# Optimization experiments

Measured on AMD Instinct MI355X. Metric: run time of the kernel, lower is better.

The kernel has to match this reference:

```python
import jax, jax.numpy as jnp
import numpy as np

N, C, T, V = 16, 128, 128, 25
K, H, OC = 3, 8, 256          # kernel_size subsets, heads, out_channels
HOPMAX = 12                   # hop values in [0, 12); emb_table size HOPMAX
EPS_BN = 1e-5
EPS_NORM = 1e-4


def setup_inputs() -> dict:
    key = jax.random.key(0)
    ks = jax.random.split(key, 12)
    s = 0.05
    x = jax.random.normal(ks[0], (N, C, T, V), jnp.float32)
    hop = jax.random.randint(ks[1], (V, V), 0, HOPMAX)
    emb_table = jax.random.normal(ks[2], (K, H, HOPMAX), jnp.float32) * s
    # A initialized as identity (as in the module) plus small noise for nontrivial grads
    A = jnp.tile(jnp.eye(V, dtype=jnp.float32), (K, H, 1, 1)) \
        + jax.random.normal(ks[3], (K, H, V, V), jnp.float32) * s
    w_block = jax.random.normal(ks[4], (K * OC, C // H), jnp.float32) * s  # grouped 1x1 conv, groups=K*H
    b_block = jax.random.normal(ks[5], (K * OC,), jnp.float32) * s
    bn_gamma = jnp.ones((OC,), jnp.float32)
    bn_beta = jnp.zeros((OC,), jnp.float32)
    res_w = jax.random.normal(ks[6], (OC, C), jnp.float32) * s  # residual 1x1 conv
    res_b = jax.random.normal(ks[7], (OC,), jnp.float32) * s
    res_bn_gamma = jnp.ones((OC,), jnp.float32)
    res_bn_beta = jnp.zeros((OC,), jnp.float32)
    return {"x": x, "hop": hop, "emb_table": emb_table, "A": A,
            "w_block": w_block, "b_block": b_block,
            "bn_gamma": bn_gamma, "bn_beta": bn_beta,
            "res_w": res_w, "res_b": res_b,
            "res_bn_gamma": res_bn_gamma, "res_bn_beta": res_bn_beta}


def _batchnorm(x, gamma, beta):
    # training-mode BatchNorm2d: batch stats over (N, T, V), biased variance
    m = jnp.mean(x, axis=(0, 2, 3), keepdims=True)
    v = jnp.var(x, axis=(0, 2, 3), keepdims=True)
    xn = (x - m) * jax.lax.rsqrt(v + EPS_BN)
    return gamma[None, :, None, None] * xn + beta[None, :, None, None]


def _l2_col_norm(w):
    # torch.norm(w, p=2, dim=-2, keepdim=True) + 1e-4  (in-degree normalization)
    return jnp.sqrt(jnp.sum(w * w, axis=-2, keepdims=True)) + EPS_NORM


def reference(x, hop, emb_table, A, w_block, b_block, bn_gamma, bn_beta,
              res_w, res_b, res_bn_gamma, res_bn_beta):
    n, c, t, v = x.shape
    # residual: 1x1 TemporalConv2d + BN (in_channels != out_channels)
    res = jnp.einsum('nctv,oc->notv', x, res_w) + res_b[None, :, None, None]
    res = _batchnorm(res, res_bn_gamma, res_bn_beta)

    # hop-embedding gather -> [K, H, V, V]; fuse normalized B and A
    B = emb_table[:, :, hop]
    BnA = B / _l2_col_norm(B) + A / _l2_col_norm(A)

    # graph conv: einsum over joint dim v (broadcast over k)
    xh = x.reshape(n, H, c // H, t, v)                      # [N,H,C/H,T,V]
    y = jnp.einsum('nhctv,khvw->nkhctw', xh, BnA)           # [N,K,H,C/H,T,V]
    y = y.reshape(n, K * H, c // H, t, v)                   # groups = K*H

    # grouped 1x1 conv: per-group [C/H -> OC/H] GEMM
    wg = w_block.reshape(K * H, OC // H, c // H)
    out = jnp.einsum('ngctv,goc->ngotv', y, wg)             # [N,K*H,OC/H,T,V]
    out = out.reshape(n, K * OC, t, v) + b_block[None, :, None, None]

    # sum over the K kernel subsets
    out = out.reshape(n, K, OC, t, v).sum(axis=1)
    out = _batchnorm(out, bn_gamma, bn_beta)
    return jax.nn.relu(out + res)
```

## Files before the change

kernel.cpp:

```cpp
#include <hip/hip_runtime.h>
#include <stdint.h>

typedef __attribute__((ext_vector_type(8))) short short8;
typedef __attribute__((ext_vector_type(4))) float f32x4;

#define B_BNA    0ull
#define B_STATS  60416ull
#define B_RESW2  64512ull
#define B_E2     1178624ull
#define B_XB     7994368ull
#define B_MAIN   21625856ull
#define B_RES    47840256ull

#define NTV 51200.0f

__device__ __forceinline__ unsigned short f2bf(float f) {
    unsigned u = __float_as_uint(f);
    return (unsigned short)((u + 0x7fffu + ((u >> 16) & 1u)) >> 16);
}
__device__ __forceinline__ float bf2f(unsigned s) { return __uint_as_float(s << 16); }

__device__ __forceinline__ float wave_sum(float v) {
#pragma unroll
    for (int m = 1; m < 64; m <<= 1) v += __shfl_xor(v, m, 64);
    return v;
}

__device__ __forceinline__ void gl_lds16(const unsigned short* g, unsigned short* l) {
    __builtin_amdgcn_global_load_lds(
        (const __attribute__((address_space(1))) unsigned int*)g,
        (__attribute__((address_space(3))) unsigned int*)l, 16, 0, 0);
}
__device__ __forceinline__ void stage_pair(const unsigned short* g0, const unsigned short* g1,
                                           unsigned short* d) {
    gl_lds16(g0, d);
    gl_lds16(g1, d + 512);
}

__device__ __forceinline__ int swz_idx(int row, int quad) {
    int rowX = row ^ ((row >> 2) & 1);
    return rowX * 32 + ((quad ^ (row & 3)) << 3);
}

__global__ __launch_bounds__(256) void k_prep(const int* __restrict__ hop,
                                              const float* __restrict__ emb,
                                              const float* __restrict__ A,
                                              const float* __restrict__ res_w,
                                              float* __restrict__ bna,
                                              float* __restrict__ stats,
                                              unsigned short* __restrict__ resw2) {
    int g = blockIdx.x, tid = threadIdx.x;
    if (g < 24) {
        if (tid < 25) {
            int w = tid;
            float nb = 0.f, na = 0.f;
            for (int v = 0; v < 25; v++) {
                float e = emb[g*12 + hop[v*25 + w]];
                nb += e*e;
                float a = A[((size_t)g*25 + v)*25 + w];
                na += a*a;
            }
            nb = sqrtf(nb) + 1e-4f;
            na = sqrtf(na) + 1e-4f;
            for (int v = 0; v < 25; v++) {
                float e = emb[g*12 + hop[v*25 + w]];
                float a = A[((size_t)g*25 + v)*25 + w];
                bna[g*625 + v*25 + w] = e/nb + a/na;
            }
        }
    } else if (g == 24) {
#pragma unroll
        for (int i = 0; i < 4; i++) stats[i*256 + tid] = 0.f;
    } else {
        int base = (g - 25) * 4096 + tid * 16;
#pragma unroll
        for (int j = 0; j < 16; j++) resw2[base + j] = f2bf(res_w[base + j]);
    }
}

__global__ __launch_bounds__(256) void k_prep2x(const float* __restrict__ w_block,
                                                const float* __restrict__ bna,
                                                unsigned short* __restrict__ E2,
                                                const float* __restrict__ x,
                                                unsigned short* __restrict__ xb) {
    int bid = blockIdx.x, tid = threadIdx.x;
    if (bid < 128) {
        __shared__ float bl[3*625];
        __shared__ float wl[3*64];
        int half = bid & 1, og = (bid >> 1) & 7, h = bid >> 4;

        for (int i = tid; i < 1875; i += 256) {
            int k3 = i / 625, j = i - k3*625;
            bl[i] = bna[(k3*8 + h)*625 + j];
        }
        if (tid < 192) {
            int k3 = tid >> 6, o = (tid >> 4) & 3, c = tid & 15;
            wl[tid] = w_block[(k3*256 + h*32 + og*4 + o)*16 + c];
        }
        __syncthreads();

        unsigned short* dst = E2 + (size_t)(h*8 + og)*53248;
        int e0 = half * 26624;
        for (int e = e0 + tid; e < e0 + 26624; e += 256) {
            int kc = e >> 12;
            int n  = (e >> 5) & 127;
            int kk = e & 31;
            int k  = kc*32 + kk;
            int o  = n >> 5, w = n & 31;
            float val = 0.f;
            if (k < 400 && w < 25) {
                int c = k / 25, v = k - c*25;
                val = wl[0*64 + o*16 + c] * bl[0*625 + v*25 + w]
                    + wl[1*64 + o*16 + c] * bl[1*625 + v*25 + w]
                    + wl[2*64 + o*16 + c] * bl[2*625 + v*25 + w];
            }
            dst[e] = f2bf(val);
        }
    } else {
        int b = bid - 128;
        int n_ = b >> 7, t_ = b & 127;
        unsigned short* row = xb + (size_t)b * 3328;
        for (int idx = tid; idx < 3200; idx += 256) {
            int c = idx / 25, v = idx - c*25;
            float val = x[(((size_t)n_*128 + c)*128 + t_)*25 + v];
            row[(c >> 4)*416 + (c & 15)*25 + v] = f2bf(val);
        }
        if (tid < 128) row[(tid >> 4)*416 + 400 + (tid & 15)] = 0;
    }
}

__global__ __launch_bounds__(256) void k_mm(const unsigned short* __restrict__ xb,
                                            const unsigned short* __restrict__ E2,
                                            unsigned short* __restrict__ mainp,
                                            const float* __restrict__ x,
                                            const unsigned short* __restrict__ resw2,
                                            unsigned short* __restrict__ resp,
                                            float* __restrict__ stats) {
    __shared__ unsigned short lds[8192];
    int bid = blockIdx.x, tid = threadIdx.x;
    int lane = tid & 63, wave = tid >> 6;
    int wm = wave >> 1, wn = wave & 1;
    int lane15 = lane & 15, quad = lane >> 4;

    if (bid < 1024) {
        int h = bid & 7, og = (bid >> 3) & 7, mt = bid >> 6;

        const unsigned short* Abase = xb + (size_t)(mt*128 + wm*64 + lane15)*3328
                                         + h*416 + quad*8;
        const unsigned short* Bbase = E2 + (size_t)(h*8 + og)*53248
                                         + (wn*64 + lane15)*32 + quad*8;

        auto loadA = [&](short8* d, int kc) {
#pragma unroll
            for (int i = 0; i < 4; i++)
                d[i] = *(const short8*)(Abase + (size_t)i*16*3328 + kc*32);
        };
        auto loadB = [&](short8* d, int kc) {
#pragma unroll
            for (int j = 0; j < 4; j++)
                d[j] = *(const short8*)(Bbase + j*512 + (size_t)kc*4096);
        };

        f32x4 acc[4][4] = {};
        short8 aA[4], bA[4], aB[4], bB[4];

        loadA(aA, 0); loadB(bA, 0);
        for (int kc = 0; kc < 13; kc += 2) {
            if (kc + 1 < 13) {
                loadA(aB, kc + 1); loadB(bB, kc + 1);
                __builtin_amdgcn_sched_barrier(0);
            }
#pragma unroll
            for (int i = 0; i < 4; i++)
#pragma unroll
                for (int j = 0; j < 4; j++)
                    acc[i][j] = __builtin_amdgcn_mfma_f32_16x16x32_bf16(aA[i], bA[j], acc[i][j], 0, 0, 0);
            if (kc + 1 < 13) {
                if (kc + 2 < 13) {
                    loadA(aA, kc + 2); loadB(bA, kc + 2);
                    __builtin_amdgcn_sched_barrier(0);
                }
#pragma unroll
                for (int i = 0; i < 4; i++)
#pragma unroll
                    for (int j = 0; j < 4; j++)
                        acc[i][j] = __builtin_amdgcn_mfma_f32_16x16x32_bf16(aB[i], bB[j], acc[i][j], 0, 0, 0);
            }
        }

        float s1[2] = {0.f, 0.f}, s2[2] = {0.f, 0.f};
#pragma unroll
        for (int j = 0; j < 4; j++) {
            int w = (j & 1)*16 + lane15;
            int p = j >> 1;
            if (w < 25) {
                int oc = h*32 + og*4 + wn*2 + p;
#pragma unroll
                for (int i = 0; i < 4; i++) {
                    int tb = wm*64 + i*16 + quad*4;
#pragma unroll
                    for (int r = 0; r < 4; r++) {
                        float val = acc[i][j][r];
                        mainp[((size_t)(mt*256 + oc)*128 + tb + r)*25 + w] = f2bf(val);
                        s1[p] += val;
                        s2[p] = fmaf(val, val, s2[p]);
                    }
                }
            }
        }
#pragma unroll
        for (int p = 0; p < 2; p++) {
            float a = wave_sum(s1[p]);
            float b = wave_sum(s2[p]);
            if (lane == 0) {
                int oc = h*32 + og*4 + wn*2 + p;
                atomicAdd(&stats[oc], a);
                atomicAdd(&stats[256 + oc], b);
            }
        }
    } else {
        int b2 = bid - 1024;
        int nt = (b2 >= 400) ? 1 : 0;
        int mt = b2 - nt*400;

        int Lrow0 = wave*32 + (lane >> 2), Lq = lane & 3;
        int r0 = Lrow0 ^ ((Lrow0 >> 2) & 1), q0 = Lq ^ (r0 & 3);
        int Lrow1 = Lrow0 + 16;
        int r1 = Lrow1 ^ ((Lrow1 >> 2) & 1), q1 = Lq ^ (r1 & 3);
        const int adoff = wave*1024 + lane*8;

        int n  = mt / 25;
        int off = (mt - n*25) * 128;
        const float* xb2 = x + (size_t)n*409600 + off;

        int c2 = tid >> 4, seg = tid & 15;

        const unsigned short* rb0 = resw2 + (size_t)(nt*128 + r0)*128 + q0*8;
        const unsigned short* rb1 = resw2 + (size_t)(nt*128 + r1)*128 + q1*8;

        f32x4 acc[4][4] = {};

        for (int kc = 0; kc < 4; kc++) {
            stage_pair(rb0 + kc*32, rb1 + kc*32, lds + 4096 + adoff);
            const float* xc0 = xb2 + (size_t)(kc*32 + 2*c2)*3200;
            const float* xc1 = xc0 + 3200;
            int wbase = 2*(c2 & 3), qn = c2 >> 2;
#pragma unroll
            for (int j = 0; j < 8; j++) {
                int m = seg + 16*j;
                unsigned pk = (unsigned)f2bf(xc0[m]) | ((unsigned)f2bf(xc1[m]) << 16);
                *(unsigned*)&lds[swz_idx(m, qn) + wbase] = pk;
            }
            __syncthreads();

            short8 af[4], bq[4];
#pragma unroll
            for (int i = 0; i < 4; i++) {
                af[i] = *(const short8*)&lds[swz_idx(wm*64 + i*16 + lane15, quad)];
                bq[i] = *(const short8*)&lds[4096 + swz_idx(wn*64 + i*16 + lane15, quad)];
            }
#pragma unroll
            for (int i = 0; i < 4; i++)
#pragma unroll
                for (int j = 0; j < 4; j++)
                    acc[i][j] = __builtin_amdgcn_mfma_f32_16x16x32_bf16(af[i], bq[j], acc[i][j], 0, 0, 0);
            __syncthreads();
        }

#pragma unroll
        for (int j = 0; j < 4; j++) {
            int oc = nt*128 + wn*64 + j*16 + lane15;
            float s1 = 0.f, s2 = 0.f;
#pragma unroll
            for (int i = 0; i < 4; i++) {
                int m2b = mt*128 + wm*64 + i*16 + quad*4;
#pragma unroll
                for (int r = 0; r < 4; r++) {
                    float val = acc[i][j][r];
                    int m2e = m2b + r;
                    int b = m2e / 25, v = m2e - b*25;
                    int nn = b >> 7, t = b & 127;
                    resp[((size_t)(nn*256 + oc)*128 + t)*25 + v] = f2bf(val);
                    s1 += val;
                    s2 = fmaf(val, val, s2);
                }
            }
            s1 += __shfl_xor(s1, 16, 64); s1 += __shfl_xor(s1, 32, 64);
            s2 += __shfl_xor(s2, 16, 64); s2 += __shfl_xor(s2, 32, 64);
            if (quad == 0) {
                atomicAdd(&stats[512 + oc], s1);
                atomicAdd(&stats[768 + oc], s2);
            }
        }
    }
}

__global__ __launch_bounds__(256) void k_final(const float* __restrict__ bn_g,
                                               const float* __restrict__ bn_b,
                                               const float* __restrict__ rbn_g,
                                               const float* __restrict__ rbn_b,
                                               const float* __restrict__ stats,
                                               const unsigned short* __restrict__ mainp,
                                               const unsigned short* __restrict__ resp,
                                               float* __restrict__ out) {
    __shared__ float4 cf[8];
    int bid = blockIdx.x, tid = threadIdx.x;
    int base_row = (bid * 1024) / 400;
    if (tid < 8) {
        int row = base_row + tid;
        if (row < 4096) {
            int oc = row & 255;
            const float inv = 1.f / NTV;
            float s1 = stats[oc],       s2 = stats[256 + oc];
            float r1v = stats[512 + oc], r2v = stats[768 + oc];
            float mm = s1*inv, vm = s2*inv - mm*mm;
            float mr = r1v*inv, vr = r2v*inv - mr*mr;
            float a1 = bn_g[oc]  * rsqrtf(vm + 1e-5f);
            float c1 = bn_b[oc]  - a1*mm;
            float a2 = rbn_g[oc] * rsqrtf(vr + 1e-5f);
            float c2 = rbn_b[oc] - a2*mr;
            cf[tid] = make_float4(a1, c1, a2, c2);
        }
    }
    __syncthreads();

    const uint4* m4 = (const uint4*)mainp;
    const uint4* r4 = (const uint4*)resp;
    float4* o4 = (float4*)out;
#pragma unroll
    for (int r = 0; r < 4; r++) {
        int chunk = bid*1024 + r*256 + tid;
        uint4 mu = m4[chunk];
        uint4 ru = r4[chunk];
        float4 C = cf[chunk/400 - base_row];
        float4 f0, f1;
        f0.x = fmaxf(fmaf(C.x, __uint_as_float(mu.x << 16),        C.y)
                   + fmaf(C.z, __uint_as_float(ru.x << 16),        C.w), 0.f);
        f0.y = fmaxf(fmaf(C.x, __uint_as_float(mu.x & 0xffff0000u), C.y)
                   + fmaf(C.z, __uint_as_float(ru.x & 0xffff0000u), C.w), 0.f);
        f0.z = fmaxf(fmaf(C.x, __uint_as_float(mu.y << 16),        C.y)
                   + fmaf(C.z, __uint_as_float(ru.y << 16),        C.w), 0.f);
        f0.w = fmaxf(fmaf(C.x, __uint_as_float(mu.y & 0xffff0000u), C.y)
                   + fmaf(C.z, __uint_as_float(ru.y & 0xffff0000u), C.w), 0.f);
        f1.x = fmaxf(fmaf(C.x, __uint_as_float(mu.z << 16),        C.y)
                   + fmaf(C.z, __uint_as_float(ru.z << 16),        C.w), 0.f);
        f1.y = fmaxf(fmaf(C.x, __uint_as_float(mu.z & 0xffff0000u), C.y)
                   + fmaf(C.z, __uint_as_float(ru.z & 0xffff0000u), C.w), 0.f);
        f1.z = fmaxf(fmaf(C.x, __uint_as_float(mu.w << 16),        C.y)
                   + fmaf(C.z, __uint_as_float(ru.w << 16),        C.w), 0.f);
        f1.w = fmaxf(fmaf(C.x, __uint_as_float(mu.w & 0xffff0000u), C.y)
                   + fmaf(C.z, __uint_as_float(ru.w & 0xffff0000u), C.w), 0.f);
        o4[chunk*2]     = f0;
        o4[chunk*2 + 1] = f1;
    }
}

extern "C" void kernel_launch(void* const* d_in, const int* in_sizes, int n_in,
                              void* d_out, int out_size, void* d_ws, size_t ws_size,
                              hipStream_t stream) {
    const float* x        = (const float*)d_in[0];
    const int*   hop      = (const int*)  d_in[1];
    const float* emb      = (const float*)d_in[2];
    const float* A        = (const float*)d_in[3];
    const float* w_block  = (const float*)d_in[4];
    const float* bn_g     = (const float*)d_in[6];
    const float* bn_b     = (const float*)d_in[7];
    const float* res_w    = (const float*)d_in[8];
    const float* rbn_g    = (const float*)d_in[10];
    const float* rbn_b    = (const float*)d_in[11];
    float* out = (float*)d_out;

    char* ws = (char*)d_ws;
    float*          bna    = (float*)(ws + B_BNA);
    float*          stats  = (float*)(ws + B_STATS);
    unsigned short* resw2  = (unsigned short*)(ws + B_RESW2);
    unsigned short* E2     = (unsigned short*)(ws + B_E2);
    unsigned short* xb     = (unsigned short*)(ws + B_XB);
    unsigned short* mainp  = (unsigned short*)(ws + B_MAIN);
    unsigned short* resp   = (unsigned short*)(ws + B_RES);

    k_prep   <<<33,   256, 0, stream>>>(hop, emb, A, res_w, bna, stats, resw2);
    k_prep2x <<<2176, 256, 0, stream>>>(w_block, bna, E2, x, xb);
    k_mm     <<<1824, 256, 0, stream>>>(xb, E2, mainp, x, resw2, resp, stats);
    k_final  <<<1600, 256, 0, stream>>>(bn_g, bn_b, rbn_g, rbn_b, stats, mainp, resp, out);
}
```

Baseline: 247.7 us.

## Fuse prep kernels and stage main GEMM through double-buffered LDS with two output groups

Merges k_prep into k_prep2x: each E2 block now computes its own normalized BnA slices in shared memory, and the stats zeroing and res_w conversion become extra blocks, which removes one launch and the bna round trip. The main GEMM path now stages A and two B tiles into double-buffered swizzled LDS via global_load_lds, and each block covers two output-channel groups. That lets the A tile be reused across both groups and halves the main-path block count from 1024 to 512. In exchange, LDS per block grows to 48KB, barriers are added each k-step, and 75 threads per block redundantly recompute the BnA normalization.

```diff
diff --git a/kernel.cpp b/kernel.cpp
--- a/kernel.cpp
+++ b/kernel.cpp
@@ -42,17 +42,25 @@
     return rowX * 32 + ((quad ^ (row & 3)) << 3);
 }
 
-__global__ __launch_bounds__(256) void k_prep(const int* __restrict__ hop,
-                                              const float* __restrict__ emb,
-                                              const float* __restrict__ A,
-                                              const float* __restrict__ res_w,
-                                              float* __restrict__ bna,
-                                              float* __restrict__ stats,
-                                              unsigned short* __restrict__ resw2) {
-    int g = blockIdx.x, tid = threadIdx.x;
-    if (g < 24) {
-        if (tid < 25) {
-            int w = tid;
+__global__ __launch_bounds__(256) void k_prep2x(const int* __restrict__ hop,
+                                                const float* __restrict__ emb,
+                                                const float* __restrict__ A,
+                                                const float* __restrict__ res_w,
+                                                const float* __restrict__ w_block,
+                                                unsigned short* __restrict__ E2,
+                                                const float* __restrict__ x,
+                                                unsigned short* __restrict__ xb,
+                                                float* __restrict__ stats,
+                                                unsigned short* __restrict__ resw2) {
+    int bid = blockIdx.x, tid = threadIdx.x;
+    if (bid < 128) {
+        __shared__ float bl[3*625];
+        __shared__ float wl[3*64];
+        int half = bid & 1, og = (bid >> 1) & 7, h = bid >> 4;
+
+        if (tid < 75) {
+            int k3 = tid / 25, w = tid - k3*25;
+            int g = k3*8 + h;
             float nb = 0.f, na = 0.f;
             for (int v = 0; v < 25; v++) {
                 float e = emb[g*12 + hop[v*25 + w]];
@@ -65,33 +73,8 @@
             for (int v = 0; v < 25; v++) {
                 float e = emb[g*12 + hop[v*25 + w]];
                 float a = A[((size_t)g*25 + v)*25 + w];
-                bna[g*625 + v*25 + w] = e/nb + a/na;
-            }
-        }
-    } else if (g == 24) {
-#pragma unroll
-        for (int i = 0; i < 4; i++) stats[i*256 + tid] = 0.f;
-    } else {
-        int base = (g - 25) * 4096 + tid * 16;
-#pragma unroll
-        for (int j = 0; j < 16; j++) resw2[base + j] = f2bf(res_w[base + j]);
-    }
-}
-
-__global__ __launch_bounds__(256) void k_prep2x(const float* __restrict__ w_block,
-                                                const float* __restrict__ bna,
-                                                unsigned short* __restrict__ E2,
-                                                const float* __restrict__ x,
-                                                unsigned short* __restrict__ xb) {
-    int bid = blockIdx.x, tid = threadIdx.x;
-    if (bid < 128) {
-        __shared__ float bl[3*625];
-        __shared__ float wl[3*64];
-        int half = bid & 1, og = (bid >> 1) & 7, h = bid >> 4;
-
-        for (int i = tid; i < 1875; i += 256) {
-            int k3 = i / 625, j = i - k3*625;
-            bl[i] = bna[(k3*8 + h)*625 + j];
+                bl[k3*625 + v*25 + w] = e/nb + a/na;
+            }
         }
         if (tid < 192) {
             int k3 = tid >> 6, o = (tid >> 4) & 3, c = tid & 15;
@@ -116,7 +99,7 @@
             }
             dst[e] = f2bf(val);
         }
-    } else {
+    } else if (bid < 2176) {
         int b = bid - 128;
         int n_ = b >> 7, t_ = b & 127;
         unsigned short* row = xb + (size_t)b * 3328;
@@ -126,108 +109,131 @@
             row[(c >> 4)*416 + (c & 15)*25 + v] = f2bf(val);
         }
         if (tid < 128) row[(tid >> 4)*416 + 400 + (tid & 15)] = 0;
+    } else if (bid == 2176) {
+#pragma unroll
+        for (int i = 0; i < 4; i++) stats[i*256 + tid] = 0.f;
+    } else {
+        int base = (bid - 2177) * 4096 + tid * 16;
+#pragma unroll
+        for (int j = 0; j < 16; j++) resw2[base + j] = f2bf(res_w[base + j]);
     }
 }
 
-__global__ __launch_bounds__(256) void k_mm(const unsigned short* __restrict__ xb,
-                                            const unsigned short* __restrict__ E2,
-                                            unsigned short* __restrict__ mainp,
-                                            const float* __restrict__ x,
-                                            const unsigned short* __restrict__ resw2,
-                                            unsigned short* __restrict__ resp,
-                                            float* __restrict__ stats) {
-    __shared__ unsigned short lds[8192];
+__global__ __launch_bounds__(256, 2) void k_mm(const unsigned short* __restrict__ xb,
+                                               const unsigned short* __restrict__ E2,
+                                               unsigned short* __restrict__ mainp,
+                                               const float* __restrict__ x,
+                                               const unsigned short* __restrict__ resw2,
+                                               unsigned short* __restrict__ resp,
+                                               float* __restrict__ stats) {
+    __shared__ unsigned short lds[24576];
     int bid = blockIdx.x, tid = threadIdx.x;
     int lane = tid & 63, wave = tid >> 6;
     int wm = wave >> 1, wn = wave & 1;
     int lane15 = lane & 15, quad = lane >> 4;
 
-    if (bid < 1024) {
-        int h = bid & 7, og = (bid >> 3) & 7, mt = bid >> 6;
-
-        const unsigned short* Abase = xb + (size_t)(mt*128 + wm*64 + lane15)*3328
-                                         + h*416 + quad*8;
-        const unsigned short* Bbase = E2 + (size_t)(h*8 + og)*53248
-                                         + (wn*64 + lane15)*32 + quad*8;
-
-        auto loadA = [&](short8* d, int kc) {
+    int Lrow0 = wave*32 + (lane >> 2), Lq = lane & 3;
+    int r0 = Lrow0 ^ ((Lrow0 >> 2) & 1), q0 = Lq ^ (r0 & 3);
+    int Lrow1 = Lrow0 + 16;
+    int r1 = Lrow1 ^ ((Lrow1 >> 2) & 1), q1 = Lq ^ (r1 & 3);
+    const int adoff = wave*1024 + lane*8;
+
+    if (bid < 512) {
+        int h = bid & 7, og2 = (bid >> 3) & 3, mt = bid >> 5;
+
+        const unsigned short* agA0 = xb + (size_t)(mt*128 + r0)*3328 + h*416 + q0*8;
+        const unsigned short* agA1 = xb + (size_t)(mt*128 + r1)*3328 + h*416 + q1*8;
+        const unsigned short* eb0  = E2 + (size_t)(h*8 + og2*2)*53248;
+        const unsigned short* eb1  = eb0 + 53248;
+        const unsigned short* b0r0 = eb0 + r0*32 + q0*8;
+        const unsigned short* b0r1 = eb0 + r1*32 + q1*8;
+        const unsigned short* b1r0 = eb1 + r0*32 + q0*8;
+        const unsigned short* b1r1 = eb1 + r1*32 + q1*8;
+
+        f32x4 acc[2][4][4] = {};
+
+        stage_pair(agA0, agA1, lds + adoff);
+        stage_pair(b0r0, b0r1, lds + 4096 + adoff);
+        stage_pair(b1r0, b1r1, lds + 8192 + adoff);
+        __syncthreads();
+
+        for (int kc = 0; kc < 13; kc++) {
+            int cur = (kc & 1) * 12288;
+            if (kc < 12) {
+                int nxt = 12288 - cur;
+                size_t ko = (size_t)(kc+1)*4096;
+                stage_pair(agA0 + (kc+1)*32, agA1 + (kc+1)*32, lds + nxt + adoff);
+                stage_pair(b0r0 + ko,        b0r1 + ko,        lds + nxt + 4096 + adoff);
+                stage_pair(b1r0 + ko,        b1r1 + ko,        lds + nxt + 8192 + adoff);
+                __builtin_amdgcn_sched_barrier(0);
+            }
+            const unsigned short* Ac  = lds + cur;
+            const unsigned short* B0c = lds + cur + 4096;
+            const unsigned short* B1c = lds + cur + 8192;
+
+            short8 af[4], bq[4];
 #pragma unroll
             for (int i = 0; i < 4; i++)
-                d[i] = *(const short8*)(Abase + (size_t)i*16*3328 + kc*32);
-        };
-        auto loadB = [&](short8* d, int kc) {
+                af[i] = *(const short8*)&Ac[swz_idx(wm*64 + i*16 + lane15, quad)];
 #pragma unroll
             for (int j = 0; j < 4; j++)
-                d[j] = *(const short8*)(Bbase + j*512 + (size_t)kc*4096);
-        };
-
-        f32x4 acc[4][4] = {};
-        short8 aA[4], bA[4], aB[4], bB[4];
-
-        loadA(aA, 0); loadB(bA, 0);
-        for (int kc = 0; kc < 13; kc += 2) {
-            if (kc + 1 < 13) {
-                loadA(aB, kc + 1); loadB(bB, kc + 1);
-                __builtin_amdgcn_sched_barrier(0);
-            }
+                bq[j] = *(const short8*)&B0c[swz_idx(wn*64 + j*16 + lane15, quad)];
 #pragma unroll
             for (int i = 0; i < 4; i++)
 #pragma unroll
                 for (int j = 0; j < 4; j++)
-                    acc[i][j] = __builtin_amdgcn_mfma_f32_16x16x32_bf16(aA[i], bA[j], acc[i][j], 0, 0, 0);
-            if (kc + 1 < 13) {
-                if (kc + 2 < 13) {
-                    loadA(aA, kc + 2); loadB(bA, kc + 2);
-                    __builtin_amdgcn_sched_barrier(0);
-                }
-#pragma unroll
-                for (int i = 0; i < 4; i++)
-#pragma unroll
-                    for (int j = 0; j < 4; j++)
-                        acc[i][j] = __builtin_amdgcn_mfma_f32_16x16x32_bf16(aB[i], bB[j], acc[i][j], 0, 0, 0);
-            }
-        }
-
-        float s1[2] = {0.f, 0.f}, s2[2] = {0.f, 0.f};
-#pragma unroll
-        for (int j = 0; j < 4; j++) {
-            int w = (j & 1)*16 + lane15;
-            int p = j >> 1;
-            if (w < 25) {
-                int oc = h*32 + og*4 + wn*2 + p;
-#pragma unroll
-                for (int i = 0; i < 4; i++) {
-                    int tb = wm*64 + i*16 + quad*4;
-#pragma unroll
-                    for (int r = 0; r < 4; r++) {
-                        float val = acc[i][j][r];
-                        mainp[((size_t)(mt*256 + oc)*128 + tb + r)*25 + w] = f2bf(val);
-                        s1[p] += val;
-                        s2[p] = fmaf(val, val, s2[p]);
+                    acc[0][i][j] = __builtin_amdgcn_mfma_f32_16x16x32_bf16(af[i], bq[j], acc[0][i][j], 0, 0, 0);
+#pragma unroll
+            for (int j = 0; j < 4; j++)
+                bq[j] = *(const short8*)&B1c[swz_idx(wn*64 + j*16 + lane15, quad)];
+#pragma unroll
+            for (int i = 0; i < 4; i++)
+#pragma unroll
+                for (int j = 0; j < 4; j++)
+                    acc[1][i][j] = __builtin_amdgcn_mfma_f32_16x16x32_bf16(af[i], bq[j], acc[1][i][j], 0, 0, 0);
+
+            if (kc < 12) __syncthreads();
+        }
+
+        float s1[2][2] = {}, s2[2][2] = {};
+#pragma unroll
+        for (int og1 = 0; og1 < 2; og1++) {
+#pragma unroll
+            for (int j = 0; j < 4; j++) {
+                int w = (j & 1)*16 + lane15;
+                int p = j >> 1;
+                if (w < 25) {
+                    int oc = h*32 + (og2*2 + og1)*4 + wn*2 + p;
+#pragma unroll
+                    for (int i = 0; i < 4; i++) {
+                        int tb = wm*64 + i*16 + quad*4;
+#pragma unroll
+                        for (int r = 0; r < 4; r++) {
+                            float val = acc[og1][i][j][r];
+                            mainp[((size_t)(mt*256 + oc)*128 + tb + r)*25 + w] = f2bf(val);
+                            s1[og1][p] += val;
+                            s2[og1][p] = fmaf(val, val, s2[og1][p]);
+                        }
                     }
                 }
             }
         }
 #pragma unroll
-        for (int p = 0; p < 2; p++) {
-            float a = wave_sum(s1[p]);
-            float b = wave_sum(s2[p]);
-            if (lane == 0) {
-                int oc = h*32 + og*4 + wn*2 + p;
-                atomicAdd(&stats[oc], a);
-                atomicAdd(&stats[256 + oc], b);
-            }
-        }
+        for (int og1 = 0; og1 < 2; og1++)
+#pragma unroll
+            for (int p = 0; p < 2; p++) {
+                float a = wave_sum(s1[og1][p]);
+                float b = wave_sum(s2[og1][p]);
+                if (lane == 0) {
+                    int oc = h*32 + (og2*2 + og1)*4 + wn*2 + p;
+                    atomicAdd(&stats[oc], a);
+                    atomicAdd(&stats[256 + oc], b);
+                }
+            }
     } else {
-        int b2 = bid - 1024;
+        int b2 = bid - 512;
         int nt = (b2 >= 400) ? 1 : 0;
         int mt = b2 - nt*400;
-
-        int Lrow0 = wave*32 + (lane >> 2), Lq = lane & 3;
-        int r0 = Lrow0 ^ ((Lrow0 >> 2) & 1), q0 = Lq ^ (r0 & 3);
-        int Lrow1 = Lrow0 + 16;
-        int r1 = Lrow1 ^ ((Lrow1 >> 2) & 1), q1 = Lq ^ (r1 & 3);
-        const int adoff = wave*1024 + lane*8;
 
         int n  = mt / 25;
         int off = (mt - n*25) * 128;
@@ -371,7 +377,6 @@
     float* out = (float*)d_out;
 
     char* ws = (char*)d_ws;
-    float*          bna    = (float*)(ws + B_BNA);
     float*          stats  = (float*)(ws + B_STATS);
     unsigned short* resw2  = (unsigned short*)(ws + B_RESW2);
     unsigned short* E2     = (unsigned short*)(ws + B_E2);
@@ -379,8 +384,7 @@
     unsigned short* mainp  = (unsigned short*)(ws + B_MAIN);
     unsigned short* resp   = (unsigned short*)(ws + B_RES);
 
-    k_prep   <<<33,   256, 0, stream>>>(hop, emb, A, res_w, bna, stats, resw2);
-    k_prep2x <<<2176, 256, 0, stream>>>(w_block, bna, E2, x, xb);
-    k_mm     <<<1824, 256, 0, stream>>>(xb, E2, mainp, x, resw2, resp, stats);
+    k_prep2x <<<2185, 256, 0, stream>>>(hop, emb, A, res_w, w_block, E2, x, xb, stats, resw2);
+    k_mm     <<<1312, 256, 0, stream>>>(xb, E2, mainp, x, resw2, resp, stats);
     k_final  <<<1600, 256, 0, stream>>>(bn_g, bn_b, rbn_g, rbn_b, stats, mainp, resp, out);
 }
```

After: 212.8 us. 1.16x faster.
